# Optimization experiments

Measured on AMD Instinct MI355X. Metric: run time of the kernel, lower is better.

The kernel has to match this reference:

```python
import jax, jax.numpy as jnp
import numpy as np

# Static conv config (matches init_kwargs)
KH, KW = 3, 3
PAD, STRIDE, DIL = 1, 1, 1


def _quantize_dynamic_int8_per_tensor(t):
    """Dynamic symmetric per-tensor int8 quantization: scale = absmax/127."""
    scale = jnp.max(jnp.abs(t)) / 127.0
    q = jnp.clip(jnp.round(t / scale), -128, 127).astype(jnp.int32)
    return q, scale


def _im2col(q, kh, kw, pad, stride, dil):
    """q: (B,C,H,W) int32 -> (B, OH*OW, C*kh*kw), torch im2col ordering (C slowest)."""
    B, C, H, W = q.shape
    OH = (H + 2 * pad - dil * (kh - 1) - 1) // stride + 1
    OW = (W + 2 * pad - dil * (kw - 1) - 1) // stride + 1
    qp = jnp.pad(q, ((0, 0), (0, 0), (pad, pad), (pad, pad)))
    row = jnp.arange(kh)[:, None] * dil + jnp.arange(OH)[None, :] * stride  # (kh, OH)
    col = jnp.arange(kw)[:, None] * dil + jnp.arange(OW)[None, :] * stride  # (kw, OW)
    # patches: (B, C, kh, kw, OH, OW)
    patches = qp[:, :, row[:, None, :, None], col[None, :, None, :]]
    patches = patches.reshape(B, C * kh * kw, OH * OW)
    return patches.transpose(0, 2, 1), OH, OW  # (B, L, C*kh*kw)


def reference(x, weight, bias, lut):
    B, C, H, W = x.shape
    O = weight.shape[0]
    # dynamic per-tensor int8 quantization of activations and weights
    qx, scale_x = _quantize_dynamic_int8_per_tensor(x)
    qw, scale_w = _quantize_dynamic_int8_per_tensor(weight)
    cols, OH, OW = _im2col(qx, KH, KW, PAD, STRIDE, DIL)  # (B, L, K)
    wmat = qw.reshape(O, -1)                               # (O, K)
    wi = wmat + 128                                        # LUT column index

    def bgemm_one(colb):  # colb: (L, K) -> (L, O) int32 via LUT multiply-accumulate
        vals = lut[colb[:, None, :] + 128, wi[None, :, :]]  # (L, O, K)
        return vals.sum(-1)

    out = jax.lax.map(bgemm_one, cols)                     # (B, L, O) int32
    out = out.astype(jnp.float32).transpose(0, 2, 1).reshape(B, O, OH, OW)
    out = out * scale_x * scale_w                          # dequantize
    out = out + bias[None, :, None, None]
    return out


def setup_inputs() -> dict:
    key = jax.random.key(0)
    k1, k2, k3 = jax.random.split(key, 3)
    x = jax.random.normal(k1, (4, 32, 32, 32), dtype=jnp.float32)
    weight = jax.random.normal(k2, (64, 32, 3, 3), dtype=jnp.float32) * 0.1
    bias = jax.random.normal(k3, (64,), dtype=jnp.float32)
    # LUT: approximate int8 multiply table indexed by (a+128, b+128).
    # Exact product table is a faithful instance of the abstraction.
    vals = np.arange(-128, 128, dtype=np.int32)
    lut = jnp.asarray(vals[:, None] * vals[None, :])  # (256, 256) int32
    return {"x": x, "weight": weight, "bias": bias, "lut": lut}
```

## Files before the change

kernel.cpp:

```cpp
#include <hip/hip_runtime.h>


#define PART_N_X 64
#define PART_N_W 8

static __device__ inline unsigned wave_umax(unsigned m) {
    #pragma unroll
    for (int off = 32; off > 0; off >>= 1) {
        unsigned o = __shfl_down(m, off, 64);
        m = m > o ? m : o;
    }
    return m;
}

static __device__ inline int dot4(unsigned a, unsigned b, int c) {
#if __has_builtin(__builtin_amdgcn_sdot4)
    return __builtin_amdgcn_sdot4((int)a, (int)b, c, false);
#else
    c += (int)(signed char)(a      ) * (int)(signed char)(b      );
    c += (int)(signed char)(a >> 8 ) * (int)(signed char)(b >> 8 );
    c += (int)(signed char)(a >> 16) * (int)(signed char)(b >> 16);
    c += (int)(signed char)(a >> 24) * (int)(signed char)(b >> 24);
    return c;
#endif
}

static __device__ inline unsigned absbits(float f) {
    return __float_as_uint(f) & 0x7fffffffu;
}

static __device__ inline unsigned quant_pack4(const float* src, int stride, float scale) {
    unsigned pk = 0u;
    #pragma unroll
    for (int j = 0; j < 4; ++j) {
        float q = rintf(src[j * stride] / scale);
        q = fminf(fmaxf(q, -128.0f), 127.0f);
        pk |= ((unsigned)((int)q & 0xff)) << (8 * j);
    }
    return pk;
}

__global__ __launch_bounds__(256) void absmax_part(const float* __restrict__ x,
                                                   const float* __restrict__ w,
                                                   unsigned* __restrict__ part) {
    int bid = blockIdx.x, tid = threadIdx.x;
    unsigned m = 0u;
    if (bid < 64) {
        const float4* p = (const float4*)x;
        int base = bid * 512;
        #pragma unroll
        for (int i = 0; i < 2; ++i) {
            float4 v = p[base + tid + i * 256];
            m = max(m, max(max(absbits(v.x), absbits(v.y)),
                           max(absbits(v.z), absbits(v.w))));
        }
    } else {
        const float4* p = (const float4*)w;
        int base = (bid - 64) * 576;
        for (int i = tid; i < 576; i += 256) {
            float4 v = p[base + i];
            m = max(m, max(max(absbits(v.x), absbits(v.y)),
                           max(absbits(v.z), absbits(v.w))));
        }
    }
    __shared__ unsigned sred[4];
    m = wave_umax(m);
    if ((tid & 63) == 0) sred[tid >> 6] = m;
    __syncthreads();
    if (tid == 0)
        part[bid] = max(max(sred[0], sred[1]), max(sred[2], sred[3]));
}

__global__ __launch_bounds__(256) void conv_fused(const float* __restrict__ x,
                                                  const float* __restrict__ w,
                                                  const float* __restrict__ bias,
                                                  const unsigned* __restrict__ part,
                                                  float* __restrict__ out) {
    int bid = blockIdx.x, tid = threadIdx.x;
    int og = bid & 15;
    int rt = (bid >> 4) & 3;
    int b  = bid >> 6;

    __shared__ unsigned xls[8 * 10 * 34];
    __shared__ unsigned wls[4 * 72];
    __shared__ float scl[2];

    {
        unsigned v = 0u;
        if (tid < PART_N_X) v = part[tid];
        else if (tid >= 64 && tid < 64 + PART_N_W) v = part[64 + (tid - 64)];
        if (tid < 128) {
            unsigned m = wave_umax(v);
            if ((tid & 63) == 0) scl[tid >> 6] = __uint_as_float(m) / 127.0f;
        }
    }
    __syncthreads();
    float sx = scl[0], sw = scl[1];

    for (int i = tid; i < 288; i += 256) {
        int o  = i / 72;
        int r  = i - o * 72;
        int c4 = r / 9;
        int kk = r - c4 * 9;
        const float* src = w + (og * 4 + o) * 288 + (c4 * 4) * 9 + kk;
        wls[i] = quant_pack4(src, 9, sw);
    }

    for (int i = tid; i < 2720; i += 256) {
        int c4  = i / 340;
        int rem = i - c4 * 340;
        int rr  = rem / 34;
        int col = rem - rr * 34;
        int ih = rt * 8 + rr - 1;
        int iw = col - 1;
        unsigned val = 0u;
        if ((unsigned)ih < 32u && (unsigned)iw < 32u) {
            const float* src = x + ((b * 32 + c4 * 4) * 32 + ih) * 32 + iw;
            val = quant_pack4(src, 1024, sx);
        }
        xls[i] = val;
    }
    __syncthreads();

    int r  = tid >> 5;
    int ow = tid & 31;
    int acc0 = 0, acc1 = 0, acc2 = 0, acc3 = 0;

    #pragma unroll
    for (int c4 = 0; c4 < 8; ++c4) {
        #pragma unroll
        for (int kh = 0; kh < 3; ++kh) {
            const unsigned* xrow = &xls[(c4 * 10 + r + kh) * 34 + ow];
            unsigned x0 = xrow[0], x1 = xrow[1], x2 = xrow[2];
            int wb = c4 * 9 + kh * 3;
            acc0 = dot4(x0, wls[0 * 72 + wb + 0], acc0);
            acc0 = dot4(x1, wls[0 * 72 + wb + 1], acc0);
            acc0 = dot4(x2, wls[0 * 72 + wb + 2], acc0);
            acc1 = dot4(x0, wls[1 * 72 + wb + 0], acc1);
            acc1 = dot4(x1, wls[1 * 72 + wb + 1], acc1);
            acc1 = dot4(x2, wls[1 * 72 + wb + 2], acc1);
            acc2 = dot4(x0, wls[2 * 72 + wb + 0], acc2);
            acc2 = dot4(x1, wls[2 * 72 + wb + 1], acc2);
            acc2 = dot4(x2, wls[2 * 72 + wb + 2], acc2);
            acc3 = dot4(x0, wls[3 * 72 + wb + 0], acc3);
            acc3 = dot4(x1, wls[3 * 72 + wb + 1], acc3);
            acc3 = dot4(x2, wls[3 * 72 + wb + 2], acc3);
        }
    }

    int oh = rt * 8 + r;
    int acc[4] = {acc0, acc1, acc2, acc3};
    #pragma unroll
    for (int oo = 0; oo < 4; ++oo) {
        int o = og * 4 + oo;
        float v = ((float)acc[oo] * sx) * sw + bias[o];
        out[((b * 64 + o) * 32 + oh) * 32 + ow] = v;
    }
}

extern "C" void kernel_launch(void* const* d_in, const int* in_sizes, int n_in,
                              void* d_out, int out_size, void* d_ws, size_t ws_size,
                              hipStream_t stream) {
    const float* x      = (const float*)d_in[0];
    const float* weight = (const float*)d_in[1];
    const float* bias   = (const float*)d_in[2];

    unsigned* part = (unsigned*)d_ws;
    float* out = (float*)d_out;

    absmax_part<<<72, 256, 0, stream>>>(x, weight, part);
    conv_fused<<<256, 256, 0, stream>>>(x, weight, bias, part, out);
}
```

Baseline: 77.09 us.

## Fuse absmax, quantization and conv into one cooperative kernel with grid syncs

Replaces the two-kernel pipeline with a single cooperative launch. Stage one computes partial absmaxes, stage two pre-quantizes x and the weights into packed int8 buffers in workspace, and stage three runs the conv, separated by grid.sync barriers. This removes one kernel launch and the redundant per-block quantization of overlapping halo data. Weights are now read from global memory instead of LDS. The cost is two grid-wide barriers plus cooperative launch overhead, and the change depends on all 256 blocks being co-resident.

```diff
diff --git a/kernel.cpp b/kernel.cpp
--- a/kernel.cpp
+++ b/kernel.cpp
@@ -1,8 +1,12 @@
 #include <hip/hip_runtime.h>
+#include <hip/hip_cooperative_groups.h>
 
+namespace cg = cooperative_groups;
 
-#define PART_N_X 64
-#define PART_N_W 8
+#define PARTX_OFF 0
+#define PARTW_OFF 256
+#define QXP_OFF   512
+#define QWP_OFF   (512 + 32768)
 
 static __device__ inline unsigned wave_umax(unsigned m) {
     #pragma unroll
@@ -25,8 +29,12 @@
 #endif
 }
 
-static __device__ inline unsigned absbits(float f) {
-    return __float_as_uint(f) & 0x7fffffffu;
+static __device__ inline unsigned abs4max(float4 v) {
+    unsigned a = __float_as_uint(v.x) & 0x7fffffffu;
+    unsigned b = __float_as_uint(v.y) & 0x7fffffffu;
+    unsigned c = __float_as_uint(v.z) & 0x7fffffffu;
+    unsigned d = __float_as_uint(v.w) & 0x7fffffffu;
+    return max(max(a, b), max(c, d));
 }
 
 static __device__ inline unsigned quant_pack4(const float* src, int stride, float scale) {
@@ -40,71 +48,72 @@
     return pk;
 }
 
-__global__ __launch_bounds__(256) void absmax_part(const float* __restrict__ x,
-                                                   const float* __restrict__ w,
-                                                   unsigned* __restrict__ part) {
+__global__ __launch_bounds__(256) void fused_all(const float* __restrict__ x,
+                                                 const float* __restrict__ w,
+                                                 const float* __restrict__ bias,
+                                                 unsigned* __restrict__ ws,
+                                                 float* __restrict__ out) {
+    cg::grid_group grid = cg::this_grid();
     int bid = blockIdx.x, tid = threadIdx.x;
-    unsigned m = 0u;
-    if (bid < 64) {
-        const float4* p = (const float4*)x;
-        int base = bid * 512;
-        #pragma unroll
-        for (int i = 0; i < 2; ++i) {
-            float4 v = p[base + tid + i * 256];
-            m = max(m, max(max(absbits(v.x), absbits(v.y)),
-                           max(absbits(v.z), absbits(v.w))));
+
+    __shared__ unsigned xls[8 * 10 * 34];
+    __shared__ unsigned rx[4], rw[4];
+    __shared__ float scl[2];
+
+    {
+        unsigned mx = 0u, mw = 0u;
+        if (tid < 128) {
+            mx = abs4max(((const float4*)x)[bid * 128 + tid]);
+        } else if (tid < 146) {
+            mw = abs4max(((const float4*)w)[bid * 18 + (tid - 128)]);
         }
-    } else {
-        const float4* p = (const float4*)w;
-        int base = (bid - 64) * 576;
-        for (int i = tid; i < 576; i += 256) {
-            float4 v = p[base + i];
-            m = max(m, max(max(absbits(v.x), absbits(v.y)),
-                           max(absbits(v.z), absbits(v.w))));
+        mx = wave_umax(mx);
+        mw = wave_umax(mw);
+        if ((tid & 63) == 0) { rx[tid >> 6] = mx; rw[tid >> 6] = mw; }
+        __syncthreads();
+        if (tid == 0) ws[PARTX_OFF + bid] = max(max(rx[0], rx[1]), max(rx[2], rx[3]));
+        if (tid == 1) ws[PARTW_OFF + bid] = max(max(rw[0], rw[1]), max(rw[2], rw[3]));
+    }
+    grid.sync();
+
+    {
+        unsigned mx = wave_umax(ws[PARTX_OFF + tid]);
+        unsigned mw = wave_umax(ws[PARTW_OFF + tid]);
+        if ((tid & 63) == 0) { rx[tid >> 6] = mx; rw[tid >> 6] = mw; }
+        __syncthreads();
+        if (tid == 0) {
+            unsigned fx = max(max(rx[0], rx[1]), max(rx[2], rx[3]));
+            unsigned fw = max(max(rw[0], rw[1]), max(rw[2], rw[3]));
+            scl[0] = __uint_as_float(fx) / 127.0f;
+            scl[1] = __uint_as_float(fw) / 127.0f;
+        }
+        __syncthreads();
+        float sx = scl[0], sw = scl[1];
+
+        if (tid < 128) {
+            int d = bid * 128 + tid;
+            int b   = d >> 13;
+            int rem = d & 8191;
+            int c4  = rem >> 10;
+            int p   = rem & 1023;
+            ws[QXP_OFF + d] = quant_pack4(x + (b * 32 + c4 * 4) * 1024 + p, 1024, sx);
+        } else if (tid < 146) {
+            int idx = bid * 18 + (tid - 128);
+            int o  = idx / 72;
+            int r  = idx - o * 72;
+            int c4 = r / 9;
+            int kk = r - c4 * 9;
+            ws[QWP_OFF + idx] = quant_pack4(w + o * 288 + c4 * 36 + kk, 9, sw);
         }
     }
-    __shared__ unsigned sred[4];
-    m = wave_umax(m);
-    if ((tid & 63) == 0) sred[tid >> 6] = m;
-    __syncthreads();
-    if (tid == 0)
-        part[bid] = max(max(sred[0], sred[1]), max(sred[2], sred[3]));
-}
+    grid.sync();
 
-__global__ __launch_bounds__(256) void conv_fused(const float* __restrict__ x,
-                                                  const float* __restrict__ w,
-                                                  const float* __restrict__ bias,
-                                                  const unsigned* __restrict__ part,
-                                                  float* __restrict__ out) {
-    int bid = blockIdx.x, tid = threadIdx.x;
+    const unsigned* qxp = ws + QXP_OFF;
+    const unsigned* qwp = ws + QWP_OFF;
+
     int og = bid & 15;
     int rt = (bid >> 4) & 3;
     int b  = bid >> 6;
-
-    __shared__ unsigned xls[8 * 10 * 34];
-    __shared__ unsigned wls[4 * 72];
-    __shared__ float scl[2];
-
-    {
-        unsigned v = 0u;
-        if (tid < PART_N_X) v = part[tid];
-        else if (tid >= 64 && tid < 64 + PART_N_W) v = part[64 + (tid - 64)];
-        if (tid < 128) {
-            unsigned m = wave_umax(v);
-            if ((tid & 63) == 0) scl[tid >> 6] = __uint_as_float(m) / 127.0f;
-        }
-    }
-    __syncthreads();
-    float sx = scl[0], sw = scl[1];
-
-    for (int i = tid; i < 288; i += 256) {
-        int o  = i / 72;
-        int r  = i - o * 72;
-        int c4 = r / 9;
-        int kk = r - c4 * 9;
-        const float* src = w + (og * 4 + o) * 288 + (c4 * 4) * 9 + kk;
-        wls[i] = quant_pack4(src, 9, sw);
-    }
 
     for (int i = tid; i < 2720; i += 256) {
         int c4  = i / 340;
@@ -114,17 +123,17 @@
         int ih = rt * 8 + rr - 1;
         int iw = col - 1;
         unsigned val = 0u;
-        if ((unsigned)ih < 32u && (unsigned)iw < 32u) {
-            const float* src = x + ((b * 32 + c4 * 4) * 32 + ih) * 32 + iw;
-            val = quant_pack4(src, 1024, sx);
-        }
+        if ((unsigned)ih < 32u && (unsigned)iw < 32u)
+            val = qxp[((b * 8 + c4) * 32 + ih) * 32 + iw];
         xls[i] = val;
     }
     __syncthreads();
 
+    float sx = scl[0], sw = scl[1];
     int r  = tid >> 5;
     int ow = tid & 31;
     int acc0 = 0, acc1 = 0, acc2 = 0, acc3 = 0;
+    const unsigned* wp = qwp + og * 4 * 72;
 
     #pragma unroll
     for (int c4 = 0; c4 < 8; ++c4) {
@@ -133,18 +142,18 @@
             const unsigned* xrow = &xls[(c4 * 10 + r + kh) * 34 + ow];
             unsigned x0 = xrow[0], x1 = xrow[1], x2 = xrow[2];
             int wb = c4 * 9 + kh * 3;
-            acc0 = dot4(x0, wls[0 * 72 + wb + 0], acc0);
-            acc0 = dot4(x1, wls[0 * 72 + wb + 1], acc0);
-            acc0 = dot4(x2, wls[0 * 72 + wb + 2], acc0);
-            acc1 = dot4(x0, wls[1 * 72 + wb + 0], acc1);
-            acc1 = dot4(x1, wls[1 * 72 + wb + 1], acc1);
-            acc1 = dot4(x2, wls[1 * 72 + wb + 2], acc1);
-            acc2 = dot4(x0, wls[2 * 72 + wb + 0], acc2);
-            acc2 = dot4(x1, wls[2 * 72 + wb + 1], acc2);
-            acc2 = dot4(x2, wls[2 * 72 + wb + 2], acc2);
-            acc3 = dot4(x0, wls[3 * 72 + wb + 0], acc3);
-            acc3 = dot4(x1, wls[3 * 72 + wb + 1], acc3);
-            acc3 = dot4(x2, wls[3 * 72 + wb + 2], acc3);
+            acc0 = dot4(x0, wp[0 * 72 + wb + 0], acc0);
+            acc0 = dot4(x1, wp[0 * 72 + wb + 1], acc0);
+            acc0 = dot4(x2, wp[0 * 72 + wb + 2], acc0);
+            acc1 = dot4(x0, wp[1 * 72 + wb + 0], acc1);
+            acc1 = dot4(x1, wp[1 * 72 + wb + 1], acc1);
+            acc1 = dot4(x2, wp[1 * 72 + wb + 2], acc1);
+            acc2 = dot4(x0, wp[2 * 72 + wb + 0], acc2);
+            acc2 = dot4(x1, wp[2 * 72 + wb + 1], acc2);
+            acc2 = dot4(x2, wp[2 * 72 + wb + 2], acc2);
+            acc3 = dot4(x0, wp[3 * 72 + wb + 0], acc3);
+            acc3 = dot4(x1, wp[3 * 72 + wb + 1], acc3);
+            acc3 = dot4(x2, wp[3 * 72 + wb + 2], acc3);
         }
     }
 
@@ -165,9 +174,10 @@
     const float* weight = (const float*)d_in[1];
     const float* bias   = (const float*)d_in[2];
 
-    unsigned* part = (unsigned*)d_ws;
+    unsigned* ws32 = (unsigned*)d_ws;
     float* out = (float*)d_out;
 
-    absmax_part<<<72, 256, 0, stream>>>(x, weight, part);
-    conv_fused<<<256, 256, 0, stream>>>(x, weight, bias, part, out);
+    void* args[] = { (void*)&x, (void*)&weight, (void*)&bias, (void*)&ws32, (void*)&out };
+    hipLaunchCooperativeKernel((const void*)fused_all, dim3(256), dim3(256),
+                               args, 0, stream);
 }
```

Result: slower. 131.4 us (+70.4%).
